# Kernel tuning notes

Hardware: AMD Instinct MI355X
Metric: run time of the kernel (lower is better)

## Reference

```python
import jax, jax.numpy as jnp
import numpy as np

EPS_DIST = 1e-10
BN_EPS = 1e-5
K = 3  # nsample / three_nn


def setup_inputs() -> dict:
    key = jax.random.key(0)
    ks = jax.random.split(key, 8)
    B, N, S, D1, D2 = 4, 8192, 2048, 128, 256
    C_in = D1 + D2  # 384
    H = 256
    inp = {
        "pos1": jax.random.normal(ks[0], (B, 3, N), dtype=jnp.float32),
        "pos2": jax.random.normal(ks[1], (B, 3, S), dtype=jnp.float32),
        "feature1": jax.random.normal(ks[2], (B, D1, N), dtype=jnp.float32),
        "feature2": jax.random.normal(ks[3], (B, D2, S), dtype=jnp.float32),
        # MLP layer 1: Conv1d(384->256, k=1) + BN
        "W1": jax.random.normal(ks[4], (H, C_in), dtype=jnp.float32) * (1.0 / np.sqrt(C_in)),
        "b1": jnp.zeros((H,), dtype=jnp.float32),
        "g1": jnp.ones((H,), dtype=jnp.float32),
        "be1": jnp.zeros((H,), dtype=jnp.float32),
        # MLP layer 2: Conv1d(256->256, k=1) + BN
        "W2": jax.random.normal(ks[5], (H, H), dtype=jnp.float32) * (1.0 / np.sqrt(H)),
        "b2": jnp.zeros((H,), dtype=jnp.float32),
        "g2": jnp.ones((H,), dtype=jnp.float32),
        "be2": jnp.zeros((H,), dtype=jnp.float32),
    }
    return inp


def _conv_bn_relu(x, W, b, gamma, beta):
    # x: [B, Cin, N]; 1x1 Conv1d == channel GEMM
    y = jnp.einsum("oc,bcn->bon", W, x) + b[None, :, None]
    # BatchNorm1d in training mode: batch statistics over (B, N)
    mean = jnp.mean(y, axis=(0, 2), keepdims=True)
    var = jnp.mean(jnp.square(y - mean), axis=(0, 2), keepdims=True)
    y = (y - mean) * jax.lax.rsqrt(var + BN_EPS)
    y = y * gamma[None, :, None] + beta[None, :, None]
    return jax.nn.relu(y)


def reference(pos1, pos2, feature1, feature2, W1, b1, g1, be1, W2, b2, g2, be2):
    # pos1: [B,3,N], pos2: [B,3,S], feature1: [B,D1,N], feature2: [B,D2,S]
    p1 = jnp.swapaxes(pos1, 1, 2)  # [B,N,3]
    p2 = jnp.swapaxes(pos2, 1, 2)  # [B,S,3]
    # three_nn: squared-distance 3-NN of each point in p1 among p2
    d2 = (jnp.sum(p1 * p1, -1)[:, :, None]
          + jnp.sum(p2 * p2, -1)[:, None, :]
          - 2.0 * jnp.einsum("bnc,bsc->bns", p1, p2))  # [B,N,S]
    neg_vals, idx = jax.lax.top_k(-d2, K)  # idx: [B,N,3]
    dists = jnp.maximum(-neg_vals, EPS_DIST)  # dists[dists<1e-10]=1e-10
    w = 1.0 / dists
    w = w / jnp.sum(w, -1, keepdims=True)  # [B,N,3]
    # grouping_operation: gather feature2 [B,D,S] by idx -> [B,D,N,3]
    grouped = jax.vmap(lambda f, i: f[:, i])(feature2, idx)
    interpolated = jnp.sum(grouped * w[:, None, :, :], axis=-1)  # [B,D2,N]
    feat = jnp.concatenate([interpolated, feature1], axis=1)  # [B,384,N]
    feat = _conv_bn_relu(feat, W1, b1, g1, be1)
    feat = _conv_bn_relu(feat, W2, b2, g2, be2)
    return feat  # [B,256,N]
```

## Files before the change

### kernel.cpp

```cpp
#include <hip/hip_runtime.h>
#include <hip/hip_bf16.h>
#include <cstdint>

typedef unsigned short u16;
typedef unsigned int u32;
typedef unsigned long long u64;
typedef __bf16 bf16x8 __attribute__((ext_vector_type(8)));
typedef float f32x4 __attribute__((ext_vector_type(4)));
typedef u16 u16x8 __attribute__((ext_vector_type(8)));

#define FPSCALE 1048576.0f
#define FPINV   (1.0f / 1048576.0f)
#define NSLICE 16

__device__ __forceinline__ u16 f2b(float f) {
    unsigned int u = __float_as_uint(f);
    u += 0x7fffu + ((u >> 16) & 1u);
    return (u16)(u >> 16);
}
__device__ __forceinline__ float b2f(u16 h) {
    return __uint_as_float(((unsigned int)h) << 16);
}
__device__ __forceinline__ void async_cp16(void* lds, const void* g) {
    __builtin_amdgcn_global_load_lds((const __attribute__((address_space(1))) void*)g,
                                     (__attribute__((address_space(3))) void*)lds, 16, 0, 0);
}
__device__ __forceinline__ u64 ld_agent_u64(const u64* p) {
    return __hip_atomic_load(p, __ATOMIC_RELAXED, __HIP_MEMORY_SCOPE_AGENT);
}
__device__ __forceinline__ u32 fmono(float f) {
    u32 u = __float_as_uint(f);
    return u ^ (((u32)((int)u >> 31)) | 0x80000000u);
}
__device__ __forceinline__ u64 shfl_xor_u64(u64 v, int mask) {
    u32 lo = (u32)v, hi = (u32)(v >> 32);
    lo = (u32)__shfl_xor((int)lo, mask);
    hi = (u32)__shfl_xor((int)hi, mask);
    return ((u64)hi << 32) | lo;
}
__device__ __forceinline__ void ins3(u64 k, u64& k0, u64& k1, u64& k2) {
    bool c0 = k > k0, c1 = k > k1, c2 = k > k2;
    k2 = c1 ? k1 : (c2 ? k : k2);
    k1 = c0 ? k0 : (c1 ? k : k1);
    k0 = c0 ? k : k0;
}
__device__ __forceinline__ int pkix(int i) { return i + (i >> 6); }

#define NB_NN  1024
#define NB_CVT 160
#define NB_T2  512
#define NB_T1  1024

__global__ __launch_bounds__(256, 6) void prep_kernel(const float* __restrict__ w1,
                                                      const float* __restrict__ w2,
                                                      u16* __restrict__ wb,
                                                      const float* __restrict__ feature2,
                                                      u16* __restrict__ f2t,
                                                      const float* __restrict__ feature1,
                                                      u16* __restrict__ f1t,
                                                      const float* __restrict__ pos1,
                                                      const float* __restrict__ pos2,
                                                      int* __restrict__ idx_out,
                                                      float* __restrict__ w_out,
                                                      u64* __restrict__ SZ) {
    __shared__ __align__(16) char smem[19712];
    int bi = blockIdx.x;
    int tid = threadIdx.x;

    if (bi >= NB_NN) {
        int ci = bi - NB_NN;
        if (ci >= NB_CVT + NB_T2 + NB_T1) {
            for (int i = tid; i < 2 * NSLICE * 512; i += 256) SZ[i] = 0;
            if (tid == 0) *(int*)(SZ + 2 * NSLICE * 512) = 0;
            return;
        }
        if (ci < NB_CVT) {
            int i = ci * 256 + tid;
            if (i < 40960) {
                const float* src = (i < 24576) ? w1 : w2;
                int k = (i < 24576) ? i : (i - 24576);
                float4 v = *(const float4*)&src[(size_t)k * 4];
                ushort4 o;
                o.x = f2b(v.x); o.y = f2b(v.y); o.z = f2b(v.z); o.w = f2b(v.w);
                *(ushort4*)&wb[(size_t)i * 4] = o;
            }
            return;
        }
        float (*t)[65] = (float (*)[65])smem;
        const float* in; u16* out; int C, S, s0, c0, b;
        if (ci < NB_CVT + NB_T2) {
            int lin = ci - NB_CVT;
            C = 256; S = 2048; in = feature2; out = f2t;
            s0 = (lin & 31) * 64; c0 = ((lin >> 5) & 3) * 64; b = lin >> 7;
        } else {
            int lin = ci - NB_CVT - NB_T2;
            C = 128; S = 8192; in = feature1; out = f1t;
            s0 = (lin & 127) * 64; c0 = ((lin >> 7) & 1) * 64; b = lin >> 8;
        }
        const float* ib = in + (size_t)b * C * S;
        u16* ob = out + (size_t)b * S * C;
        int col = tid & 63, r0 = tid >> 6;
#pragma unroll
        for (int p = 0; p < 16; ++p) {
            int c = p * 4 + r0;
            t[c][col] = ib[(size_t)(c0 + c) * S + s0 + col];
        }
        __syncthreads();
#pragma unroll
        for (int p = 0; p < 16; ++p) {
            int s = p * 4 + r0;
            ob[(size_t)(s0 + s) * C + c0 + col] = f2b(t[col][s]);
        }
        return;
    }

    float4* pk = (float4*)smem;
    u64* warr = (u64*)(smem + 16640);
    int j0 = bi * 32;
    int b = j0 >> 13;
    const float* p2 = pos2 + (size_t)b * 3 * 2048;
    int p = tid & 15, ck = tid >> 4;
    int wv = tid >> 6, lane = tid & 63;
    const float* p1 = pos1 + (size_t)b * 3 * 8192;
    float qx[2], qy[2], qz[2];
#pragma unroll
    for (int t = 0; t < 2; ++t) {
        int n = (j0 & 8191) + p + t * 16;
        qx[t] = p1[n]; qy[t] = p1[8192 + n]; qz[t] = p1[16384 + n];
    }
    u64 key[2][3];
#pragma unroll
    for (int t = 0; t < 2; ++t) { key[t][0] = 0; key[t][1] = 0; key[t][2] = 0; }

    for (int half = 0; half < 2; ++half) {
        int hbase = half * 1024;
        for (int i = tid; i < 1024; i += 256) {
            int s = hbase + i;
            float x = p2[s], y = p2[2048 + s], z = p2[4096 + s];
            pk[pkix(i)] = make_float4(x, y, z, -0.5f * (x * x + y * y + z * z));
        }
        __syncthreads();

        float g[2][3]; int id[2][3];
#pragma unroll
        for (int t = 0; t < 2; ++t) {
            g[t][0] = -3.4e38f; g[t][1] = -3.4e38f; g[t][2] = -3.4e38f;
            id[t][0] = 0; id[t][1] = 0; id[t][2] = 0;
        }
        int sb = ck * 64;
        const float4* pc = pk + pkix(sb);
#pragma unroll 2
        for (int it = 0; it < 64; ++it) {
            float4 cd = pc[it];
            int s = sb + it;
#pragma unroll
            for (int t = 0; t < 2; ++t) {
                float tv = fmaf(qx[t], cd.x, fmaf(qy[t], cd.y, fmaf(qz[t], cd.z, cd.w)));
                bool c0 = tv > g[t][0], c1 = tv > g[t][1], c2 = tv > g[t][2];
                float o0 = g[t][0], o1 = g[t][1];
                g[t][2] = __builtin_amdgcn_fmed3f(tv, o1, g[t][2]);
                g[t][1] = __builtin_amdgcn_fmed3f(tv, o0, o1);
                g[t][0] = fmaxf(o0, tv);
                id[t][2] = c1 ? id[t][1] : (c2 ? s : id[t][2]);
                id[t][1] = c0 ? id[t][0] : (c1 ? s : id[t][1]);
                id[t][0] = c0 ? s : id[t][0];
            }
        }
        __syncthreads();

#pragma unroll
        for (int t = 0; t < 2; ++t) {
#pragma unroll
            for (int r = 0; r < 3; ++r)
                ins3(((u64)fmono(g[t][r]) << 32) | (u64)(2047 - (hbase + id[t][r])),
                     key[t][0], key[t][1], key[t][2]);
        }
    }

#pragma unroll
    for (int mask = 16; mask <= 32; mask <<= 1) {
#pragma unroll
        for (int t = 0; t < 2; ++t) {
            u64 m0 = shfl_xor_u64(key[t][0], mask);
            u64 m1 = shfl_xor_u64(key[t][1], mask);
            u64 m2 = shfl_xor_u64(key[t][2], mask);
            ins3(m0, key[t][0], key[t][1], key[t][2]);
            ins3(m1, key[t][0], key[t][1], key[t][2]);
            ins3(m2, key[t][0], key[t][1], key[t][2]);
        }
    }
    if (lane < 16) {
        u64* wr = &warr[(wv * 16 + p) * 6];
#pragma unroll
        for (int t = 0; t < 2; ++t) {
            wr[t * 3 + 0] = key[t][0]; wr[t * 3 + 1] = key[t][1]; wr[t * 3 + 2] = key[t][2];
        }
    }
    __syncthreads();
    if (tid < 32) {
        int pp = tid & 15, t = tid >> 4;
        const u64* w0 = &warr[pp * 6 + t * 3];
        u64 k0 = w0[0], k1 = w0[1], k2 = w0[2];
#pragma unroll
        for (int w = 1; w < 4; ++w) {
            const u64* wr = &warr[(w * 16 + pp) * 6 + t * 3];
            ins3(wr[0], k0, k1, k2);
            ins3(wr[1], k0, k1, k2);
            ins3(wr[2], k0, k1, k2);
        }
        int s0 = 2047 - (int)(k0 & 0xFFFFFFFFu);
        int s1 = 2047 - (int)(k1 & 0xFFFFFFFFu);
        int s2 = 2047 - (int)(k2 & 0xFFFFFFFFu);
        int j = j0 + pp + t * 16;
        int n = j & 8191;
        float x1 = p1[n], y1 = p1[8192 + n], z1 = p1[16384 + n];
        float n1 = x1 * x1 + y1 * y1 + z1 * z1;
        float X0 = p2[s0], Y0 = p2[2048 + s0], Z0 = p2[4096 + s0];
        float X1 = p2[s1], Y1v = p2[2048 + s1], Z1 = p2[4096 + s1];
        float X2 = p2[s2], Y2v = p2[2048 + s2], Z2 = p2[4096 + s2];
        float t0 = x1 * X0 + y1 * Y0 + z1 * Z0 - 0.5f * (X0 * X0 + Y0 * Y0 + Z0 * Z0);
        float t1 = x1 * X1 + y1 * Y1v + z1 * Z1 - 0.5f * (X1 * X1 + Y1v * Y1v + Z1 * Z1);
        float t2 = x1 * X2 + y1 * Y2v + z1 * Z2 - 0.5f * (X2 * X2 + Y2v * Y2v + Z2 * Z2);
        float d0 = fmaxf(fmaf(-2.f, t0, n1), 1e-10f);
        float d1 = fmaxf(fmaf(-2.f, t1, n1), 1e-10f);
        float d2 = fmaxf(fmaf(-2.f, t2, n1), 1e-10f);
        float w0v = 1.f / d0, w1v = 1.f / d1, w2v = 1.f / d2;
        float inv = 1.f / (w0v + w1v + w2v);
        idx_out[j * 3] = s0; idx_out[j * 3 + 1] = s1; idx_out[j * 3 + 2] = s2;
        w_out[j * 3] = w0v * inv; w_out[j * 3 + 1] = w1v * inv; w_out[j * 3 + 2] = w2v * inv;
    }
}

__global__ __launch_bounds__(256, 8) void interp_kernel(const u16* __restrict__ f2t,
                                                        const int* __restrict__ idx,
                                                        const float* __restrict__ wgt,
                                                        u16* __restrict__ out) {
    int tid = threadIdx.x;
    int j = blockIdx.x * 16 + (tid >> 4);
    int c0 = (tid & 15) * 16;
    int b = j >> 13;
    const u16* fb = f2t + (size_t)b * 2048 * 256;
    const u16* r0 = fb + (size_t)idx[j * 3 + 0] * 256 + c0;
    const u16* r1 = fb + (size_t)idx[j * 3 + 1] * 256 + c0;
    const u16* r2 = fb + (size_t)idx[j * 3 + 2] * 256 + c0;
    float w0 = wgt[j * 3 + 0], w1 = wgt[j * 3 + 1], w2 = wgt[j * 3 + 2];
    u16* ob = out + (size_t)j * 256 + c0;
#pragma unroll
    for (int cc = 0; cc < 2; ++cc) {
        u16x8 v0 = *(const u16x8*)(r0 + cc * 8);
        u16x8 v1 = *(const u16x8*)(r1 + cc * 8);
        u16x8 v2 = *(const u16x8*)(r2 + cc * 8);
        u16x8 o;
#pragma unroll
        for (int e = 0; e < 8; ++e)
            o[e] = f2b(w0 * b2f(v0[e]) + w1 * b2f(v1[e]) + w2 * b2f(v2[e]));
        *(u16x8*)(ob + cc * 8) = o;
    }
}

__global__ __launch_bounds__(256, 2) void gemm1_kernel(const u16* __restrict__ A1,
                                                       const u16* __restrict__ A2,
                                                       const u16* __restrict__ Bw,
                                                       const float* __restrict__ bias,
                                                       u16* __restrict__ Yb,
                                                       u64* __restrict__ S1) {
    __shared__ __align__(16) char smemA[36864];
    u16* Al = (u16*)smemA;
    u16* Bl = (u16*)(smemA + 16384);
    u16* T  = (u16*)smemA;
    int tid = threadIdx.x;
    int lane = tid & 63, wv = tid >> 6;
    int j0 = blockIdx.x * 128, m0 = blockIdx.y * 128;
    int l15 = lane & 15, q = lane >> 4;
    int wj = (wv >> 1) * 64, wm = (wv & 1) * 64;
    f32x4 acc[4][4];
#pragma unroll
    for (int i = 0; i < 4; ++i)
#pragma unroll
        for (int jj = 0; jj < 4; ++jj) acc[i][jj] = (f32x4){0.f, 0.f, 0.f, 0.f};

    int rbase = wv * 32;
    int lrow = lane >> 3, lchunk = lane & 7;
    int schunk = lchunk ^ lrow;
    const u16* Bg = Bw + (size_t)m0 * 384;

    for (int k0 = 0; k0 < 384; k0 += 64) {
#pragma unroll
        for (int qq = 0; qq < 4; ++qq) {
            int row = rbase + qq * 8;
            async_cp16(&Bl[row * 64], Bg + (size_t)(row + lrow) * 384 + k0 + schunk * 8);
        }
        const u16* src; int str;
        if (k0 < 256) { src = A1 + (size_t)j0 * 256 + k0;         str = 256; }
        else          { src = A2 + (size_t)j0 * 128 + (k0 - 256); str = 128; }
#pragma unroll
        for (int qq = 0; qq < 4; ++qq) {
            int row = rbase + qq * 8;
            async_cp16(&Al[row * 64], src + (size_t)(row + lrow) * str + schunk * 8);
        }
        __syncthreads();
#pragma unroll
        for (int ks = 0; ks < 2; ++ks) {
            bf16x8 af[4], bfr[4];
#pragma unroll
            for (int i = 0; i < 4; ++i) {
                int row = wj + i * 16 + l15;
                af[i] = *(const bf16x8*)&Al[row * 64 + ((ks * 4 + q) ^ (l15 & 7)) * 8];
            }
#pragma unroll
            for (int i = 0; i < 4; ++i) {
                int row = wm + i * 16 + l15;
                bfr[i] = *(const bf16x8*)&Bl[row * 64 + ((ks * 4 + q) ^ (l15 & 7)) * 8];
            }
#pragma unroll
            for (int i = 0; i < 4; ++i)
#pragma unroll
                for (int jj = 0; jj < 4; ++jj)
                    acc[i][jj] = __builtin_amdgcn_mfma_f32_16x16x32_bf16(af[i], bfr[jj],
                                                                         acc[i][jj], 0, 0, 0);
        }
        __syncthreads();
    }
    int sl = (blockIdx.x & (NSLICE - 1)) * 512;
#pragma unroll
    for (int jj = 0; jj < 4; ++jj) {
        int ml = wm + jj * 16 + l15;
        float bv = bias[m0 + ml];
        float s = 0.f, s2 = 0.f;
#pragma unroll
        for (int i = 0; i < 4; ++i) {
            int jl = wj + i * 16 + q * 4;
#pragma unroll
            for (int r = 0; r < 4; ++r) {
                float v = acc[i][jj][r] + bv;
                s += v; s2 += v * v;
                T[(jl + r) * 136 + ml] = f2b(v);
            }
        }
        s += __shfl_xor(s, 16); s += __shfl_xor(s, 32);
        s2 += __shfl_xor(s2, 16); s2 += __shfl_xor(s2, 32);
        if (q == 0) {
            atomicAdd(&S1[sl + m0 + ml], (u64)(long long)llrintf(s * FPSCALE));
            atomicAdd(&S1[sl + 256 + m0 + ml], (u64)(long long)llrintf(s2 * FPSCALE));
        }
    }
    __syncthreads();
#pragma unroll
    for (int it = 0; it < 8; ++it) {
        int jl = it * 16 + wv * 4 + q;
        u16x8 v = *(const u16x8*)&T[jl * 136 + l15 * 8];
        *(u16x8*)&Yb[(size_t)(j0 + jl) * 256 + m0 + l15 * 8] = v;
    }
}

__device__ __forceinline__ void gridbar(int* cnt, int target) {
    __syncthreads();
    if (threadIdx.x == 0) {
        __hip_atomic_fetch_add(cnt, 1, __ATOMIC_RELAXED, __HIP_MEMORY_SCOPE_AGENT);
        while (__hip_atomic_load(cnt, __ATOMIC_RELAXED, __HIP_MEMORY_SCOPE_AGENT) < target)
            __builtin_amdgcn_s_sleep(16);
        __atomic_signal_fence(__ATOMIC_SEQ_CST);
    }
    __syncthreads();
}

__global__ __launch_bounds__(256, 2) void gemm2_fused(const u16* __restrict__ Y1,
                                                      const u16* __restrict__ Bw,
                                                      const float* __restrict__ bias,
                                                      const u64* __restrict__ S1,
                                                      const float* __restrict__ g1,
                                                      const float* __restrict__ be1,
                                                      u64* __restrict__ S2,
                                                      const float* __restrict__ g2,
                                                      const float* __restrict__ be2,
                                                      float* __restrict__ OUT,
                                                      int* __restrict__ BAR) {
    __shared__ __align__(16) char smemA[36864];
    u16* Al = (u16*)smemA;
    u16* Bl = (u16*)(smemA + 16384);
    u16* T  = (u16*)smemA;
    float2* BNT = (float2*)(smemA + 34816);
    int tid = threadIdx.x;
    int bid = blockIdx.x;
    int lane = tid & 63, wv = tid >> 6;
    int j0 = (bid >> 1) * 128, m0 = (bid & 1) * 128;
    int l15 = lane & 15, q = lane >> 4;
    int wj = (wv >> 1) * 64, wm = (wv & 1) * 64;

    {
        long long su = 0, sq = 0;
#pragma unroll
        for (int r = 0; r < NSLICE; ++r) {
            su += (long long)S1[r * 512 + tid];
            sq += (long long)S1[r * 512 + 256 + tid];
        }
        float fs  = (float)su * FPINV;
        float fs2 = (float)sq * FPINV;
        const float inv = 1.f / 32768.f;
        float mean = fs * inv;
        float var = fs2 * inv - mean * mean;
        float a = g1[tid] * rsqrtf(var + 1e-5f);
        BNT[tid] = make_float2(a, be1[tid] - mean * a);
    }
    __syncthreads();

    f32x4 acc[4][4];
#pragma unroll
    for (int i = 0; i < 4; ++i)
#pragma unroll
        for (int jj = 0; jj < 4; ++jj) acc[i][jj] = (f32x4){0.f, 0.f, 0.f, 0.f};

    int rbase = wv * 32;
    int lrow = lane >> 3, lchunk = lane & 7;
    int schunk = lchunk ^ lrow;
    const u16* Bg = Bw + (size_t)m0 * 256;

    for (int k0 = 0; k0 < 256; k0 += 64) {
#pragma unroll
        for (int qq = 0; qq < 4; ++qq) {
            int row = rbase + qq * 8;
            async_cp16(&Bl[row * 64], Bg + (size_t)(row + lrow) * 256 + k0 + schunk * 8);
        }
        int c = k0 + lchunk * 8;
        float2 bn[8];
#pragma unroll
        for (int e = 0; e < 8; ++e) bn[e] = BNT[c + e];
#pragma unroll
        for (int qq = 0; qq < 4; ++qq) {
            int row = rbase + qq * 8;
            u16x8 y = *(const u16x8*)&Y1[(size_t)(j0 + row + lrow) * 256 + c];
            u16x8 o;
#pragma unroll
            for (int e = 0; e < 8; ++e)
                o[e] = f2b(fmaxf(b2f(y[e]) * bn[e].x + bn[e].y, 0.f));
            *(u16x8*)&Al[(row + lrow) * 64 + schunk * 8] = o;
        }
        __syncthreads();
#pragma unroll
        for (int ks = 0; ks < 2; ++ks) {
            bf16x8 af[4], bfr[4];
#pragma unroll
            for (int i = 0; i < 4; ++i) {
                int row = wj + i * 16 + l15;
                af[i] = *(const bf16x8*)&Al[row * 64 + ((ks * 4 + q) ^ (l15 & 7)) * 8];
            }
#pragma unroll
            for (int i = 0; i < 4; ++i) {
                int row = wm + i * 16 + l15;
                bfr[i] = *(const bf16x8*)&Bl[row * 64 + ((ks * 4 + q) ^ (l15 & 7)) * 8];
            }
#pragma unroll
            for (int i = 0; i < 4; ++i)
#pragma unroll
                for (int jj = 0; jj < 4; ++jj)
                    acc[i][jj] = __builtin_amdgcn_mfma_f32_16x16x32_bf16(af[i], bfr[jj],
                                                                         acc[i][jj], 0, 0, 0);
        }
        __syncthreads();
    }

    int sl2 = ((bid >> 1) & (NSLICE - 1)) * 512;
#pragma unroll
    for (int jj = 0; jj < 4; ++jj) {
        int ml = wm + jj * 16 + l15;
        float bv = bias[m0 + ml];
        float s = 0.f, s2 = 0.f;
#pragma unroll
        for (int i = 0; i < 4; ++i) {
            int jl = wj + i * 16 + q * 4;
#pragma unroll
            for (int r = 0; r < 4; ++r) {
                float v = acc[i][jj][r] + bv;
                s += v; s2 += v * v;
                T[ml * 136 + (jl + r)] = f2b(v);
            }
        }
        s += __shfl_xor(s, 16); s += __shfl_xor(s, 32);
        s2 += __shfl_xor(s2, 16); s2 += __shfl_xor(s2, 32);
        if (q == 0) {
            atomicAdd(&S2[sl2 + m0 + ml], (u64)(long long)llrintf(s * FPSCALE));
            atomicAdd(&S2[sl2 + 256 + m0 + ml], (u64)(long long)llrintf(s2 * FPSCALE));
        }
    }
    gridbar(BAR, 512);

    if (tid < 128) {
        int c = m0 + tid;
        long long su = 0, sq = 0;
#pragma unroll
        for (int r = 0; r < NSLICE; ++r) {
            su += (long long)ld_agent_u64(&S2[r * 512 + c]);
            sq += (long long)ld_agent_u64(&S2[r * 512 + 256 + c]);
        }
        float fs  = (float)su * FPINV;
        float fs2 = (float)sq * FPINV;
        const float inv = 1.f / 32768.f;
        float mean = fs * inv;
        float var = fs2 * inv - mean * mean;
        float a = g2[c] * rsqrtf(var + 1e-5f);
        BNT[tid] = make_float2(a, be2[c] - mean * a);
    }
    __syncthreads();

    int ol8 = tid >> 5;
    int j4 = (tid & 31) * 4;
    int bb = j0 >> 13, n0 = j0 & 8191;
#pragma unroll
    for (int it = 0; it < 16; ++it) {
        int ol = it * 8 + ol8;
        float2 bn = BNT[ol];
        ushort4 h = *(const ushort4*)&T[ol * 136 + j4];
        float4 v;
        v.x = fmaxf(b2f(h.x) * bn.x + bn.y, 0.f);
        v.y = fmaxf(b2f(h.y) * bn.x + bn.y, 0.f);
        v.z = fmaxf(b2f(h.z) * bn.x + bn.y, 0.f);
        v.w = fmaxf(b2f(h.w) * bn.x + bn.y, 0.f);
        *(float4*)&OUT[(size_t)bb * 2097152 + (size_t)(m0 + ol) * 8192 + n0 + j4] = v;
    }
}

extern "C" void kernel_launch(void* const* d_in, const int* in_sizes, int n_in,
                              void* d_out, int out_size, void* d_ws, size_t ws_size,
                              hipStream_t stream) {
    const float* pos1 = (const float*)d_in[0];
    const float* pos2 = (const float*)d_in[1];
    const float* feature1 = (const float*)d_in[2];
    const float* feature2 = (const float*)d_in[3];
    const float* W1 = (const float*)d_in[4];
    const float* b1 = (const float*)d_in[5];
    const float* g1 = (const float*)d_in[6];
    const float* be1 = (const float*)d_in[7];
    const float* W2 = (const float*)d_in[8];
    const float* b2 = (const float*)d_in[9];
    const float* g2 = (const float*)d_in[10];
    const float* be2 = (const float*)d_in[11];

    char* ws = (char*)d_ws;
    int*    IDX   = (int*)(ws + 0);
    float*  WGT   = (float*)(ws + 393216);
    u16*    W1B   = (u16*)(ws + 786432);
    u16*    W2B   = (u16*)(ws + 983040);
    u16*    F2T   = (u16*)(ws + 1118208);
    u16*    F1T   = (u16*)(ws + 5312512);
    u16*    Y1    = (u16*)(ws + 13701120);
    u16*    INTERP= (u16*)(ws + 30478336);
    u64*    SSTAT = (u64*)(ws + 47255552);
    u64*    S1    = SSTAT;
    u64*    S2    = SSTAT + NSLICE * 512;
    int*    BAR   = (int*)(SSTAT + 2 * NSLICE * 512);
    float*  OUT   = (float*)d_out;

    prep_kernel<<<NB_NN + NB_CVT + NB_T2 + NB_T1 + 1, 256, 0, stream>>>(
        W1, W2, W1B, feature2, F2T, feature1, F1T, pos1, pos2, IDX, WGT, SSTAT);
    interp_kernel<<<2048, 256, 0, stream>>>(F2T, IDX, WGT, INTERP);
    gemm1_kernel<<<dim3(256, 2), 256, 0, stream>>>(INTERP, F1T, W1B, b1, Y1, S1);
    gemm2_fused<<<512, 256, 0, stream>>>(Y1, W2B, b2, S1, g1, be1,
                                         S2, g2, be2, OUT, BAR);
}
```

Baseline: 188.4 us.

## Fuse both MLP GEMMs into one persistent kernel and narrow NN blocks

Replaces the separate gemm1 and gemm2 kernels with a single persistent kernel of 256 blocks. Each block computes all 256 output channels for 128 points. The layer-1 result stays in registers and LDS, and grid barriers synchronize the two BatchNorm statistic reductions. This removes the Y1 round trip through global memory and one kernel launch. Per-block partial sums are first reduced in LDS, which cuts the number of global atomics. Separately, the 3-NN search now gives each thread one query instead of two and launches twice as many blocks at higher occupancy. The costs are one block per CU with large LDS use, and a grid barrier that relies on all 256 blocks being co-resident.

Result: faster. 183.2 us (-2.8%).

```diff
diff --git a/kernel.cpp b/kernel.cpp
--- a/kernel.cpp
+++ b/kernel.cpp
@@ -46,12 +46,12 @@
 }
 __device__ __forceinline__ int pkix(int i) { return i + (i >> 6); }
 
-#define NB_NN  1024
+#define NB_NN  2048
 #define NB_CVT 160
 #define NB_T2  512
 #define NB_T1  1024
 
-__global__ __launch_bounds__(256, 6) void prep_kernel(const float* __restrict__ w1,
+__global__ __launch_bounds__(256, 8) void prep_kernel(const float* __restrict__ w1,
                                                       const float* __restrict__ w2,
                                                       u16* __restrict__ wb,
                                                       const float* __restrict__ feature2,
@@ -63,7 +63,7 @@
                                                       int* __restrict__ idx_out,
                                                       float* __restrict__ w_out,
                                                       u64* __restrict__ SZ) {
-    __shared__ __align__(16) char smem[19712];
+    __shared__ __align__(16) char smem[18176];
     int bi = blockIdx.x;
     int tid = threadIdx.x;
 
@@ -116,21 +116,15 @@
 
     float4* pk = (float4*)smem;
     u64* warr = (u64*)(smem + 16640);
-    int j0 = bi * 32;
+    int j0 = bi * 16;
     int b = j0 >> 13;
     const float* p2 = pos2 + (size_t)b * 3 * 2048;
     int p = tid & 15, ck = tid >> 4;
     int wv = tid >> 6, lane = tid & 63;
     const float* p1 = pos1 + (size_t)b * 3 * 8192;
-    float qx[2], qy[2], qz[2];
-#pragma unroll
-    for (int t = 0; t < 2; ++t) {
-        int n = (j0 & 8191) + p + t * 16;
-        qx[t] = p1[n]; qy[t] = p1[8192 + n]; qz[t] = p1[16384 + n];
-    }
-    u64 key[2][3];
-#pragma unroll
-    for (int t = 0; t < 2; ++t) { key[t][0] = 0; key[t][1] = 0; key[t][2] = 0; }
+    int n = (j0 & 8191) + p;
+    float qx = p1[n], qy = p1[8192 + n], qz = p1[16384 + n];
+    u64 key0 = 0, key1 = 0, key2 = 0;
 
     for (int half = 0; half < 2; ++half) {
         int hbase = half * 1024;
@@ -141,69 +135,52 @@
         }
         __syncthreads();
 
-        float g[2][3]; int id[2][3];
-#pragma unroll
-        for (int t = 0; t < 2; ++t) {
-            g[t][0] = -3.4e38f; g[t][1] = -3.4e38f; g[t][2] = -3.4e38f;
-            id[t][0] = 0; id[t][1] = 0; id[t][2] = 0;
-        }
+        float g0 = -3.4e38f, g1 = -3.4e38f, g2 = -3.4e38f;
+        int id0 = 0, id1 = 0, id2 = 0;
         int sb = ck * 64;
         const float4* pc = pk + pkix(sb);
-#pragma unroll 2
+#pragma unroll 4
         for (int it = 0; it < 64; ++it) {
             float4 cd = pc[it];
             int s = sb + it;
-#pragma unroll
-            for (int t = 0; t < 2; ++t) {
-                float tv = fmaf(qx[t], cd.x, fmaf(qy[t], cd.y, fmaf(qz[t], cd.z, cd.w)));
-                bool c0 = tv > g[t][0], c1 = tv > g[t][1], c2 = tv > g[t][2];
-                float o0 = g[t][0], o1 = g[t][1];
-                g[t][2] = __builtin_amdgcn_fmed3f(tv, o1, g[t][2]);
-                g[t][1] = __builtin_amdgcn_fmed3f(tv, o0, o1);
-                g[t][0] = fmaxf(o0, tv);
-                id[t][2] = c1 ? id[t][1] : (c2 ? s : id[t][2]);
-                id[t][1] = c0 ? id[t][0] : (c1 ? s : id[t][1]);
-                id[t][0] = c0 ? s : id[t][0];
-            }
-        }
-        __syncthreads();
-
-#pragma unroll
-        for (int t = 0; t < 2; ++t) {
-#pragma unroll
-            for (int r = 0; r < 3; ++r)
-                ins3(((u64)fmono(g[t][r]) << 32) | (u64)(2047 - (hbase + id[t][r])),
-                     key[t][0], key[t][1], key[t][2]);
-        }
+            float tv = fmaf(qx, cd.x, fmaf(qy, cd.y, fmaf(qz, cd.z, cd.w)));
+            bool c0 = tv > g0, c1 = tv > g1, c2 = tv > g2;
+            float o0 = g0, o1 = g1;
+            g2 = __builtin_amdgcn_fmed3f(tv, o1, g2);
+            g1 = __builtin_amdgcn_fmed3f(tv, o0, o1);
+            g0 = fmaxf(o0, tv);
+            id2 = c1 ? id1 : (c2 ? s : id2);
+            id1 = c0 ? id0 : (c1 ? s : id1);
+            id0 = c0 ? s : id0;
+        }
+        __syncthreads();
+
+        ins3(((u64)fmono(g0) << 32) | (u64)(2047 - (hbase + id0)), key0, key1, key2);
+        ins3(((u64)fmono(g1) << 32) | (u64)(2047 - (hbase + id1)), key0, key1, key2);
+        ins3(((u64)fmono(g2) << 32) | (u64)(2047 - (hbase + id2)), key0, key1, key2);
     }
 
 #pragma unroll
     for (int mask = 16; mask <= 32; mask <<= 1) {
-#pragma unroll
-        for (int t = 0; t < 2; ++t) {
-            u64 m0 = shfl_xor_u64(key[t][0], mask);
-            u64 m1 = shfl_xor_u64(key[t][1], mask);
-            u64 m2 = shfl_xor_u64(key[t][2], mask);
-            ins3(m0, key[t][0], key[t][1], key[t][2]);
-            ins3(m1, key[t][0], key[t][1], key[t][2]);
-            ins3(m2, key[t][0], key[t][1], key[t][2]);
-        }
+        u64 m0 = shfl_xor_u64(key0, mask);
+        u64 m1 = shfl_xor_u64(key1, mask);
+        u64 m2 = shfl_xor_u64(key2, mask);
+        ins3(m0, key0, key1, key2);
+        ins3(m1, key0, key1, key2);
+        ins3(m2, key0, key1, key2);
     }
     if (lane < 16) {
-        u64* wr = &warr[(wv * 16 + p) * 6];
-#pragma unroll
-        for (int t = 0; t < 2; ++t) {
-            wr[t * 3 + 0] = key[t][0]; wr[t * 3 + 1] = key[t][1]; wr[t * 3 + 2] = key[t][2];
-        }
-    }
-    __syncthreads();
-    if (tid < 32) {
-        int pp = tid & 15, t = tid >> 4;
-        const u64* w0 = &warr[pp * 6 + t * 3];
+        u64* wr = &warr[(wv * 16 + p) * 3];
+        wr[0] = key0; wr[1] = key1; wr[2] = key2;
+    }
+    __syncthreads();
+    if (tid < 16) {
+        int pp = tid;
+        const u64* w0 = &warr[pp * 3];
         u64 k0 = w0[0], k1 = w0[1], k2 = w0[2];
 #pragma unroll
         for (int w = 1; w < 4; ++w) {
-            const u64* wr = &warr[(w * 16 + pp) * 6 + t * 3];
+            const u64* wr = &warr[(w * 16 + pp) * 3];
             ins3(wr[0], k0, k1, k2);
             ins3(wr[1], k0, k1, k2);
             ins3(wr[2], k0, k1, k2);
@@ -211,9 +188,9 @@
         int s0 = 2047 - (int)(k0 & 0xFFFFFFFFu);
         int s1 = 2047 - (int)(k1 & 0xFFFFFFFFu);
         int s2 = 2047 - (int)(k2 & 0xFFFFFFFFu);
-        int j = j0 + pp + t * 16;
-        int n = j & 8191;
-        float x1 = p1[n], y1 = p1[8192 + n], z1 = p1[16384 + n];
+        int j = j0 + pp;
+        int nn = j & 8191;
+        float x1 = p1[nn], y1 = p1[8192 + nn], z1 = p1[16384 + nn];
         float n1 = x1 * x1 + y1 * y1 + z1 * z1;
         float X0 = p2[s0], Y0 = p2[2048 + s0], Z0 = p2[4096 + s0];
         float X1 = p2[s1], Y1v = p2[2048 + s1], Z1 = p2[4096 + s1];
@@ -258,101 +235,6 @@
     }
 }
 
-__global__ __launch_bounds__(256, 2) void gemm1_kernel(const u16* __restrict__ A1,
-                                                       const u16* __restrict__ A2,
-                                                       const u16* __restrict__ Bw,
-                                                       const float* __restrict__ bias,
-                                                       u16* __restrict__ Yb,
-                                                       u64* __restrict__ S1) {
-    __shared__ __align__(16) char smemA[36864];
-    u16* Al = (u16*)smemA;
-    u16* Bl = (u16*)(smemA + 16384);
-    u16* T  = (u16*)smemA;
-    int tid = threadIdx.x;
-    int lane = tid & 63, wv = tid >> 6;
-    int j0 = blockIdx.x * 128, m0 = blockIdx.y * 128;
-    int l15 = lane & 15, q = lane >> 4;
-    int wj = (wv >> 1) * 64, wm = (wv & 1) * 64;
-    f32x4 acc[4][4];
-#pragma unroll
-    for (int i = 0; i < 4; ++i)
-#pragma unroll
-        for (int jj = 0; jj < 4; ++jj) acc[i][jj] = (f32x4){0.f, 0.f, 0.f, 0.f};
-
-    int rbase = wv * 32;
-    int lrow = lane >> 3, lchunk = lane & 7;
-    int schunk = lchunk ^ lrow;
-    const u16* Bg = Bw + (size_t)m0 * 384;
-
-    for (int k0 = 0; k0 < 384; k0 += 64) {
-#pragma unroll
-        for (int qq = 0; qq < 4; ++qq) {
-            int row = rbase + qq * 8;
-            async_cp16(&Bl[row * 64], Bg + (size_t)(row + lrow) * 384 + k0 + schunk * 8);
-        }
-        const u16* src; int str;
-        if (k0 < 256) { src = A1 + (size_t)j0 * 256 + k0;         str = 256; }
-        else          { src = A2 + (size_t)j0 * 128 + (k0 - 256); str = 128; }
-#pragma unroll
-        for (int qq = 0; qq < 4; ++qq) {
-            int row = rbase + qq * 8;
-            async_cp16(&Al[row * 64], src + (size_t)(row + lrow) * str + schunk * 8);
-        }
-        __syncthreads();
-#pragma unroll
-        for (int ks = 0; ks < 2; ++ks) {
-            bf16x8 af[4], bfr[4];
-#pragma unroll
-            for (int i = 0; i < 4; ++i) {
-                int row = wj + i * 16 + l15;
-                af[i] = *(const bf16x8*)&Al[row * 64 + ((ks * 4 + q) ^ (l15 & 7)) * 8];
-            }
-#pragma unroll
-            for (int i = 0; i < 4; ++i) {
-                int row = wm + i * 16 + l15;
-                bfr[i] = *(const bf16x8*)&Bl[row * 64 + ((ks * 4 + q) ^ (l15 & 7)) * 8];
-            }
-#pragma unroll
-            for (int i = 0; i < 4; ++i)
-#pragma unroll
-                for (int jj = 0; jj < 4; ++jj)
-                    acc[i][jj] = __builtin_amdgcn_mfma_f32_16x16x32_bf16(af[i], bfr[jj],
-                                                                         acc[i][jj], 0, 0, 0);
-        }
-        __syncthreads();
-    }
-    int sl = (blockIdx.x & (NSLICE - 1)) * 512;
-#pragma unroll
-    for (int jj = 0; jj < 4; ++jj) {
-        int ml = wm + jj * 16 + l15;
-        float bv = bias[m0 + ml];
-        float s = 0.f, s2 = 0.f;
-#pragma unroll
-        for (int i = 0; i < 4; ++i) {
-            int jl = wj + i * 16 + q * 4;
-#pragma unroll
-            for (int r = 0; r < 4; ++r) {
-                float v = acc[i][jj][r] + bv;
-                s += v; s2 += v * v;
-                T[(jl + r) * 136 + ml] = f2b(v);
-            }
-        }
-        s += __shfl_xor(s, 16); s += __shfl_xor(s, 32);
-        s2 += __shfl_xor(s2, 16); s2 += __shfl_xor(s2, 32);
-        if (q == 0) {
-            atomicAdd(&S1[sl + m0 + ml], (u64)(long long)llrintf(s * FPSCALE));
-            atomicAdd(&S1[sl + 256 + m0 + ml], (u64)(long long)llrintf(s2 * FPSCALE));
-        }
-    }
-    __syncthreads();
-#pragma unroll
-    for (int it = 0; it < 8; ++it) {
-        int jl = it * 16 + wv * 4 + q;
-        u16x8 v = *(const u16x8*)&T[jl * 136 + l15 * 8];
-        *(u16x8*)&Yb[(size_t)(j0 + jl) * 256 + m0 + l15 * 8] = v;
-    }
-}
-
 __device__ __forceinline__ void gridbar(int* cnt, int target) {
     __syncthreads();
     if (threadIdx.x == 0) {
@@ -364,37 +246,115 @@
     __syncthreads();
 }
 
-__global__ __launch_bounds__(256, 2) void gemm2_fused(const u16* __restrict__ Y1,
-                                                      const u16* __restrict__ Bw,
-                                                      const float* __restrict__ bias,
-                                                      const u64* __restrict__ S1,
-                                                      const float* __restrict__ g1,
-                                                      const float* __restrict__ be1,
-                                                      u64* __restrict__ S2,
-                                                      const float* __restrict__ g2,
-                                                      const float* __restrict__ be2,
-                                                      float* __restrict__ OUT,
-                                                      int* __restrict__ BAR) {
-    __shared__ __align__(16) char smemA[36864];
-    u16* Al = (u16*)smemA;
-    u16* Bl = (u16*)(smemA + 16384);
-    u16* T  = (u16*)smemA;
-    float2* BNT = (float2*)(smemA + 34816);
-    int tid = threadIdx.x;
-    int bid = blockIdx.x;
+__global__ __launch_bounds__(256, 1) void mlp_fused(const u16* __restrict__ A1,
+                                                    const u16* __restrict__ A2g,
+                                                    const u16* __restrict__ W1b,
+                                                    const float* __restrict__ b1,
+                                                    const u16* __restrict__ W2b,
+                                                    const float* __restrict__ b2,
+                                                    u64* __restrict__ S1,
+                                                    const float* __restrict__ g1,
+                                                    const float* __restrict__ be1,
+                                                    u64* __restrict__ S2,
+                                                    const float* __restrict__ g2,
+                                                    const float* __restrict__ be2,
+                                                    float* __restrict__ OUT,
+                                                    int* __restrict__ BAR) {
+    __shared__ __align__(16) char smem[98304];
+    u16* AS  = (u16*)smem;
+    u16* BS  = (u16*)(smem + 16384);
+    u16* A2  = (u16*)smem;
+    u16* BS2 = (u16*)(smem + 65536);
+    float* SC  = (float*)(smem + 65536);
+    float* SC2 = (float*)(smem + 65536 + 4096);
+    float2* BNT = (float2*)(smem + 65536);
+
+    int tid = threadIdx.x, bid = blockIdx.x;
     int lane = tid & 63, wv = tid >> 6;
-    int j0 = (bid >> 1) * 128, m0 = (bid & 1) * 128;
     int l15 = lane & 15, q = lane >> 4;
-    int wj = (wv >> 1) * 64, wm = (wv & 1) * 64;
+    int lrow = lane >> 3, lchunk = lane & 7, schunk = lchunk ^ lrow;
+    int j0 = bid * 128;
+    int wrow = wv * 32;
+    int sl = (bid & (NSLICE - 1)) * 512;
+
+    f32x4 acc[2][16];
+#pragma unroll
+    for (int i = 0; i < 2; ++i)
+#pragma unroll
+        for (int jj = 0; jj < 16; ++jj) acc[i][jj] = (f32x4){0.f, 0.f, 0.f, 0.f};
+
+    for (int k0 = 0; k0 < 384; k0 += 64) {
+#pragma unroll
+        for (int qq = 0; qq < 8; ++qq) {
+            int row = wv * 64 + qq * 8;
+            async_cp16(&BS[row * 64], W1b + (size_t)(row + lrow) * 384 + k0 + schunk * 8);
+        }
+        const u16* src; int str;
+        if (k0 < 256) { src = A1 + (size_t)j0 * 256 + k0;          str = 256; }
+        else          { src = A2g + (size_t)j0 * 128 + (k0 - 256); str = 128; }
+#pragma unroll
+        for (int qq = 0; qq < 4; ++qq) {
+            int row = wv * 32 + qq * 8;
+            async_cp16(&AS[row * 64], src + (size_t)(row + lrow) * str + schunk * 8);
+        }
+        __syncthreads();
+#pragma unroll
+        for (int ks = 0; ks < 2; ++ks) {
+            bf16x8 af[2];
+#pragma unroll
+            for (int i = 0; i < 2; ++i) {
+                int row = wrow + i * 16 + l15;
+                af[i] = *(const bf16x8*)&AS[row * 64 + ((ks * 4 + q) ^ (l15 & 7)) * 8];
+            }
+#pragma unroll
+            for (int jj = 0; jj < 16; ++jj) {
+                int row = jj * 16 + l15;
+                bf16x8 bfr = *(const bf16x8*)&BS[row * 64 + ((ks * 4 + q) ^ (l15 & 7)) * 8];
+#pragma unroll
+                for (int i = 0; i < 2; ++i)
+                    acc[i][jj] = __builtin_amdgcn_mfma_f32_16x16x32_bf16(af[i], bfr,
+                                                                         acc[i][jj], 0, 0, 0);
+            }
+        }
+        __syncthreads();
+    }
+
+#pragma unroll
+    for (int jj = 0; jj < 16; ++jj) {
+        float bv = b1[jj * 16 + l15];
+        float s = 0.f, s2 = 0.f;
+#pragma unroll
+        for (int i = 0; i < 2; ++i)
+#pragma unroll
+            for (int r = 0; r < 4; ++r) {
+                acc[i][jj][r] += bv;
+                float v = acc[i][jj][r];
+                s += v; s2 += v * v;
+            }
+        s += __shfl_xor(s, 16); s += __shfl_xor(s, 32);
+        s2 += __shfl_xor(s2, 16); s2 += __shfl_xor(s2, 32);
+        if (q == 0) {
+            SC[wv * 256 + jj * 16 + l15] = s;
+            SC2[wv * 256 + jj * 16 + l15] = s2;
+        }
+    }
+    __syncthreads();
+    {
+        float fs = SC[tid] + SC[256 + tid] + SC[512 + tid] + SC[768 + tid];
+        float fs2 = SC2[tid] + SC2[256 + tid] + SC2[512 + tid] + SC2[768 + tid];
+        atomicAdd(&S1[sl + tid], (u64)(long long)llrintf(fs * FPSCALE));
+        atomicAdd(&S1[sl + 256 + tid], (u64)(long long)llrintf(fs2 * FPSCALE));
+    }
+    gridbar(BAR, 256);
 
     {
         long long su = 0, sq = 0;
 #pragma unroll
         for (int r = 0; r < NSLICE; ++r) {
-            su += (long long)S1[r * 512 + tid];
-            sq += (long long)S1[r * 512 + 256 + tid];
-        }
-        float fs  = (float)su * FPINV;
+            su += (long long)ld_agent_u64(&S1[r * 512 + tid]);
+            sq += (long long)ld_agent_u64(&S1[r * 512 + 256 + tid]);
+        }
+        float fs = (float)su * FPINV;
         float fs2 = (float)sq * FPINV;
         const float inv = 1.f / 32768.f;
         float mean = fs * inv;
@@ -404,119 +364,119 @@
     }
     __syncthreads();
 
-    f32x4 acc[4][4];
-#pragma unroll
-    for (int i = 0; i < 4; ++i)
-#pragma unroll
-        for (int jj = 0; jj < 4; ++jj) acc[i][jj] = (f32x4){0.f, 0.f, 0.f, 0.f};
-
-    int rbase = wv * 32;
-    int lrow = lane >> 3, lchunk = lane & 7;
-    int schunk = lchunk ^ lrow;
-    const u16* Bg = Bw + (size_t)m0 * 256;
-
-    for (int k0 = 0; k0 < 256; k0 += 64) {
-#pragma unroll
-        for (int qq = 0; qq < 4; ++qq) {
-            int row = rbase + qq * 8;
-            async_cp16(&Bl[row * 64], Bg + (size_t)(row + lrow) * 256 + k0 + schunk * 8);
-        }
-        int c = k0 + lchunk * 8;
-        float2 bn[8];
-#pragma unroll
-        for (int e = 0; e < 8; ++e) bn[e] = BNT[c + e];
-#pragma unroll
-        for (int qq = 0; qq < 4; ++qq) {
-            int row = rbase + qq * 8;
-            u16x8 y = *(const u16x8*)&Y1[(size_t)(j0 + row + lrow) * 256 + c];
-            u16x8 o;
-#pragma unroll
-            for (int e = 0; e < 8; ++e)
-                o[e] = f2b(fmaxf(b2f(y[e]) * bn[e].x + bn[e].y, 0.f));
-            *(u16x8*)&Al[(row + lrow) * 64 + schunk * 8] = o;
+#pragma unroll
+    for (int i = 0; i < 2; ++i)
+#pragma unroll
+        for (int jj = 0; jj < 16; ++jj) {
+            int c = jj * 16 + l15;
+            float2 bn = BNT[c];
+            int chunkbase = c >> 3;
+            int win = c & 7;
+#pragma unroll
+            for (int r = 0; r < 4; ++r) {
+                int row = wrow + i * 16 + q * 4 + r;
+                float vb = b2f(f2b(acc[i][jj][r]));
+                u16 h = f2b(fmaxf(vb * bn.x + bn.y, 0.f));
+                A2[row * 256 + ((chunkbase ^ (row & 7)) * 8 + win)] = h;
+            }
+        }
+    __syncthreads();
+
+#pragma unroll
+    for (int i = 0; i < 2; ++i)
+#pragma unroll
+        for (int jj = 0; jj < 16; ++jj) acc[i][jj] = (f32x4){0.f, 0.f, 0.f, 0.f};
+
+    for (int kstep = 0; kstep < 4; ++kstep) {
+        int k0 = kstep * 64;
+#pragma unroll
+        for (int qq = 0; qq < 8; ++qq) {
+            int row = wv * 64 + qq * 8;
+            async_cp16(&BS2[row * 64], W2b + (size_t)(row + lrow) * 256 + k0 + schunk * 8);
         }
         __syncthreads();
 #pragma unroll
         for (int ks = 0; ks < 2; ++ks) {
-            bf16x8 af[4], bfr[4];
-#pragma unroll
-            for (int i = 0; i < 4; ++i) {
-                int row = wj + i * 16 + l15;
-                af[i] = *(const bf16x8*)&Al[row * 64 + ((ks * 4 + q) ^ (l15 & 7)) * 8];
-            }
-#pragma unroll
-            for (int i = 0; i < 4; ++i) {
-                int row = wm + i * 16 + l15;
-                bfr[i] = *(const bf16x8*)&Bl[row * 64 + ((ks * 4 + q) ^ (l15 & 7)) * 8];
-            }
-#pragma unroll
-            for (int i = 0; i < 4; ++i)
-#pragma unroll
-                for (int jj = 0; jj < 4; ++jj)
-                    acc[i][jj] = __builtin_amdgcn_mfma_f32_16x16x32_bf16(af[i], bfr[jj],
+            bf16x8 af[2];
+#pragma unroll
+            for (int i = 0; i < 2; ++i) {
+                int row = wrow + i * 16 + l15;
+                int kc = kstep * 8 + ks * 4 + q;
+                af[i] = *(const bf16x8*)&A2[row * 256 + ((kc ^ (row & 7)) * 8)];
+            }
+#pragma unroll
+            for (int jj = 0; jj < 16; ++jj) {
+                int row = jj * 16 + l15;
+                bf16x8 bfr = *(const bf16x8*)&BS2[row * 64 + ((ks * 4 + q) ^ (l15 & 7)) * 8];
+#pragma unroll
+                for (int i = 0; i < 2; ++i)
+                    acc[i][jj] = __builtin_amdgcn_mfma_f32_16x16x32_bf16(af[i], bfr,
                                                                          acc[i][jj], 0, 0, 0);
-        }
-        __syncthreads();
-    }
-
-    int sl2 = ((bid >> 1) & (NSLICE - 1)) * 512;
-#pragma unroll
-    for (int jj = 0; jj < 4; ++jj) {
-        int ml = wm + jj * 16 + l15;
-        float bv = bias[m0 + ml];
+            }
+        }
+        __syncthreads();
+    }
+
+#pragma unroll
+    for (int jj = 0; jj < 16; ++jj) {
+        float bv = b2[jj * 16 + l15];
         float s = 0.f, s2 = 0.f;
 #pragma unroll
-        for (int i = 0; i < 4; ++i) {
-            int jl = wj + i * 16 + q * 4;
+        for (int i = 0; i < 2; ++i)
 #pragma unroll
             for (int r = 0; r < 4; ++r) {
-                float v = acc[i][jj][r] + bv;
+                acc[i][jj][r] += bv;
+                float v = acc[i][jj][r];
                 s += v; s2 += v * v;
-                T[ml * 136 + (jl + r)] = f2b(v);
-            }
-        }
+            }
         s += __shfl_xor(s, 16); s += __shfl_xor(s, 32);
         s2 += __shfl_xor(s2, 16); s2 += __shfl_xor(s2, 32);
         if (q == 0) {
-            atomicAdd(&S2[sl2 + m0 + ml], (u64)(long long)llrintf(s * FPSCALE));
-            atomicAdd(&S2[sl2 + 256 + m0 + ml], (u64)(long long)llrintf(s2 * FPSCALE));
-        }
+            SC[wv * 256 + jj * 16 + l15] = s;
+            SC2[wv * 256 + jj * 16 + l15] = s2;
+        }
+    }
+    __syncthreads();
+    {
+        float fs = SC[tid] + SC[256 + tid] + SC[512 + tid] + SC[768 + tid];
+        float fs2 = SC2[tid] + SC2[256 + tid] + SC2[512 + tid] + SC2[768 + tid];
+        atomicAdd(&S2[sl + tid], (u64)(long long)llrintf(fs * FPSCALE));
+        atomicAdd(&S2[sl + 256 + tid], (u64)(long long)llrintf(fs2 * FPSCALE));
     }
     gridbar(BAR, 512);
 
-    if (tid < 128) {
-        int c = m0 + tid;
+    {
         long long su = 0, sq = 0;
 #pragma unroll
         for (int r = 0; r < NSLICE; ++r) {
-            su += (long long)ld_agent_u64(&S2[r * 512 + c]);
-            sq += (long long)ld_agent_u64(&S2[r * 512 + 256 + c]);
-        }
-        float fs  = (float)su * FPINV;
+            su += (long long)ld_agent_u64(&S2[r * 512 + tid]);
+            sq += (long long)ld_agent_u64(&S2[r * 512 + 256 + tid]);
+        }
+        float fs = (float)su * FPINV;
         float fs2 = (float)sq * FPINV;
         const float inv = 1.f / 32768.f;
         float mean = fs * inv;
         float var = fs2 * inv - mean * mean;
-        float a = g2[c] * rsqrtf(var + 1e-5f);
-        BNT[tid] = make_float2(a, be2[c] - mean * a);
-    }
-    __syncthreads();
-
-    int ol8 = tid >> 5;
-    int j4 = (tid & 31) * 4;
-    int bb = j0 >> 13, n0 = j0 & 8191;
-#pragma unroll
-    for (int it = 0; it < 16; ++it) {
-        int ol = it * 8 + ol8;
-        float2 bn = BNT[ol];
-        ushort4 h = *(const ushort4*)&T[ol * 136 + j4];
-        float4 v;
-        v.x = fmaxf(b2f(h.x) * bn.x + bn.y, 0.f);
-        v.y = fmaxf(b2f(h.y) * bn.x + bn.y, 0.f);
-        v.z = fmaxf(b2f(h.z) * bn.x + bn.y, 0.f);
-        v.w = fmaxf(b2f(h.w) * bn.x + bn.y, 0.f);
-        *(float4*)&OUT[(size_t)bb * 2097152 + (size_t)(m0 + ol) * 8192 + n0 + j4] = v;
-    }
+        float a = g2[tid] * rsqrtf(var + 1e-5f);
+        BNT[tid] = make_float2(a, be2[tid] - mean * a);
+    }
+    __syncthreads();
+
+    int bb = j0 >> 13, nbase = j0 & 8191;
+#pragma unroll
+    for (int i = 0; i < 2; ++i)
+#pragma unroll
+        for (int jj = 0; jj < 16; ++jj) {
+            int o = jj * 16 + l15;
+            float2 bn = BNT[o];
+            int n0 = nbase + wrow + i * 16 + q * 4;
+            float4 v;
+            v.x = fmaxf(b2f(f2b(acc[i][jj][0])) * bn.x + bn.y, 0.f);
+            v.y = fmaxf(b2f(f2b(acc[i][jj][1])) * bn.x + bn.y, 0.f);
+            v.z = fmaxf(b2f(f2b(acc[i][jj][2])) * bn.x + bn.y, 0.f);
+            v.w = fmaxf(b2f(f2b(acc[i][jj][3])) * bn.x + bn.y, 0.f);
+            *(float4*)&OUT[(size_t)bb * 2097152 + (size_t)o * 8192 + n0] = v;
+        }
 }
 
 extern "C" void kernel_launch(void* const* d_in, const int* in_sizes, int n_in,
@@ -542,7 +502,6 @@
     u16*    W2B   = (u16*)(ws + 983040);
     u16*    F2T   = (u16*)(ws + 1118208);
     u16*    F1T   = (u16*)(ws + 5312512);
-    u16*    Y1    = (u16*)(ws + 13701120);
     u16*    INTERP= (u16*)(ws + 30478336);
     u64*    SSTAT = (u64*)(ws + 47255552);
     u64*    S1    = SSTAT;
@@ -553,7 +512,6 @@
     prep_kernel<<<NB_NN + NB_CVT + NB_T2 + NB_T1 + 1, 256, 0, stream>>>(
         W1, W2, W1B, feature2, F2T, feature1, F1T, pos1, pos2, IDX, WGT, SSTAT);
     interp_kernel<<<2048, 256, 0, stream>>>(F2T, IDX, WGT, INTERP);
-    gemm1_kernel<<<dim3(256, 2), 256, 0, stream>>>(INTERP, F1T, W1B, b1, Y1, S1);
-    gemm2_fused<<<512, 256, 0, stream>>>(Y1, W2B, b2, S1, g1, be1,
-                                         S2, g2, be2, OUT, BAR);
-}
+    mlp_fused<<<256, 256, 0, stream>>>(INTERP, F1T, W1B, b1, W2B, b2,
+                                       S1, g1, be1, S2, g2, be2, OUT, BAR);
+}
```
